# Performance work log

Hardware: AMD Instinct MI355X
Metric: run time of the kernel (lower is better)

Reference implementation:

```python
import jax, jax.numpy as jnp
import numpy as np

B, C, H, W = 4, 64, 128, 128
G, K, PAD, DIL = 4, 3, 2, 2  # deformable conv config
OFF_CH = 2 * K * K * G  # 72


def conv2d(x, w, b, pad):
    out = jax.lax.conv_general_dilated(
        x, w, window_strides=(1, 1), padding=[(pad, pad), (pad, pad)],
        dimension_numbers=('NCHW', 'OIHW', 'NCHW'))
    return out + b[None, :, None, None]


def deform_conv(x, offset, w, b):
    # DCNv1 (no modulation mask), groups=G, offset_groups=G, torchvision semantics.
    Bn, Cn, Hn, Wn = x.shape
    Cg = Cn // G
    Cout = w.shape[0]
    Coutg = Cout // G
    # offset channels laid out as [G, K*K, (dy,dx)]
    off = offset.reshape(Bn, G, K * K, 2, Hn, Wn)
    dy, dx = off[:, :, :, 0], off[:, :, :, 1]  # [B,G,9,H,W]
    kk = jnp.arange(K * K)
    gy = (jnp.arange(Hn)[None, :] - PAD + DIL * (kk // K)[:, None]).astype(x.dtype)[:, :, None]  # [9,H,1]
    gx = (jnp.arange(Wn)[None, :] - PAD + DIL * (kk % K)[:, None]).astype(x.dtype)[:, None, :]   # [9,1,W]
    py = dy + gy[None, None]  # [B,G,9,H,W]
    px = dx + gx[None, None]
    xg = x.reshape(Bn, G, Cg, Hn, Wn)

    def gather(img, py_, px_):  # img [Cg,H,W]; py_,px_ [9,H,W]
        y0 = jnp.floor(py_)
        x0 = jnp.floor(px_)
        ly = py_ - y0
        lx = px_ - x0

        def corner(iy, ix, wgt):
            valid = (iy >= 0) & (iy <= Hn - 1) & (ix >= 0) & (ix <= Wn - 1)
            iyc = jnp.clip(iy, 0, Hn - 1).astype(jnp.int32)
            ixc = jnp.clip(ix, 0, Wn - 1).astype(jnp.int32)
            return img[:, iyc, ixc] * (wgt * valid)[None]

        return (corner(y0, x0, (1 - ly) * (1 - lx))
                + corner(y0, x0 + 1, (1 - ly) * lx)
                + corner(y0 + 1, x0, ly * (1 - lx))
                + corner(y0 + 1, x0 + 1, ly * lx))

    sampled = jax.vmap(jax.vmap(gather))(xg, py, px)  # [B,G,Cg,9,H,W]
    wr = w.reshape(G, Coutg, Cg, K * K)
    out = jnp.einsum('bgckhw,gock->bgohw', sampled, wr).reshape(Bn, Cout, Hn, Wn)
    return out + b[None, :, None, None]


def setup_inputs() -> dict:
    key = jax.random.key(0)
    ks = jax.random.split(key, 32)
    f32 = jnp.float32
    d = {
        'Fref': jax.random.normal(ks[0], (B, C, H, W), f32),
        'Fmov1': jax.random.normal(ks[1], (B, C, H, W), f32),
        'Fmov2': jax.random.normal(ks[2], (B, C, H, W), f32),
        'cr_w': jax.random.normal(ks[3], (64, 128, 3, 3), f32) * 0.05,
        'cr_b': jax.random.normal(ks[4], (64,), f32) * 0.05,
    }
    i = 5
    for name in ('off1', 'off2', 'off3', 'off4'):
        d[name + '_w'] = jax.random.normal(ks[i], (OFF_CH, 64, 3, 3), f32) * 0.01
        d[name + '_b'] = jax.random.normal(ks[i + 1], (OFF_CH,), f32) * 0.01
        i += 2
    for name in ('d1', 'd2', 'd3', 'd4'):
        d[name + '_w'] = jax.random.normal(ks[i], (64, 64 // G, 3, 3), f32) * 0.05
        d[name + '_b'] = jax.random.normal(ks[i + 1], (64,), f32) * 0.05
        i += 2
    return d


def reference(Fref, Fmov1, Fmov2, cr_w, cr_b,
              off1_w, off1_b, off2_w, off2_b, off3_w, off3_b, off4_w, off4_b,
              d1_w, d1_b, d2_w, d2_b, d3_w, d3_b, d4_w, d4_b):
    def align(fr, fm):
        fea = conv2d(jnp.concatenate([fr, fm], axis=1), cr_w, cr_b, 1)
        fea = deform_conv(fea, conv2d(fea, off1_w, off1_b, 1), d1_w, d1_b)
        fea = deform_conv(fea, conv2d(fea, off2_w, off2_b, 1), d2_w, d2_b)
        off3 = conv2d(fea, off3_w, off3_b, 1)
        fea = deform_conv(fm, off3, d3_w, d3_b)  # note: deform3 applied to Fmov, per source
        out = deform_conv(fea, conv2d(fea, off4_w, off4_b, 1), d4_w, d4_b)
        return out

    return (align(Fref, Fmov1), align(Fref, Fmov2))
```

## Files before the change

kernel.cpp:

```cpp
#include <hip/hip_runtime.h>


using f16   = _Float16;
using f16x8 = __attribute__((ext_vector_type(8))) f16;
using h2    = __attribute__((ext_vector_type(2))) f16;
using u16x8 = __attribute__((ext_vector_type(8))) unsigned short;
using f32x4 = __attribute__((ext_vector_type(4))) float;

static constexpr int Hh = 128, Ww = 128, NB = 4, NPIX = Hh * Ww;
static constexpr int BB = 8;

__device__ __forceinline__ unsigned short f2h(float f) {
  f16 h = (f16)f;
  return *(unsigned short*)&h;
}

struct PrepPtrs {
  const float* cw[5];
  unsigned short* cd[5];
  const float* dw[4];
  unsigned short* dd[4];
  const float* ob[4];
  float* obd[4];
};

__global__ __launch_bounds__(256) void prep_all_kernel(PrepPtrs pp) {
  const int which = blockIdx.y;
  const int i = blockIdx.x * 256 + threadIdx.x;
  if (which == 0) {
    if (i >= 9 * 64 * 128) return;
    const int cin = 128, cop = 64;
    const int ci = i % cin, co = (i / cin) % cop, t = i / (cin * cop);
    pp.cd[0][i] = f2h(pp.cw[0][((size_t)co * cin + ci) * 9 + t]);
  } else if (which <= 4) {
    if (i >= 9 * 80 * 64) return;
    const int cin = 64, cop = 80;
    const int ci = i % cin, co = (i / cin) % cop, t = i / (cin * cop);
    const int g = co / 20, c = co % 20;
    float v = (c < 18) ? pp.cw[which][((size_t)(g * 18 + c) * cin + ci) * 9 + t]
                       : 0.f;
    pp.cd[which][i] = f2h(v);
  } else if (which <= 8) {
    if (i >= 4 * 5 * 16 * 32) return;
    const int kk = i & 31, o = (i >> 5) & 15, pair = (i >> 9) % 5;
    const int g = i / 2560;
    const int t = pair * 2 + (kk >> 4), c = kk & 15;
    float v = (t < 9) ? pp.dw[which - 5][(size_t)((g * 16 + o) * 16 + c) * 9 + t]
                      : 0.f;
    pp.dd[which - 5][i] = f2h(v);
  } else {
    if (i >= 4 * 80) return;
    const int ten = i / 80, co = i % 80;
    const int g = co / 20, c = co % 20;
    pp.obd[ten][co] = (c < 18) ? pp.ob[ten][g * 18 + c] : 0.f;
  }
}

__global__ __launch_bounds__(256) void to_gs_kernel(
    const float* __restrict__ Fref, const float* __restrict__ Fm1,
    const float* __restrict__ Fm2, unsigned short* __restrict__ frefG,
    unsigned short* __restrict__ fmovG) {
  const int t = blockIdx.x * 256 + threadIdx.x;
  const int b2 = t >> 14, pix = t & (NPIX - 1);
  const float* fm = (b2 < 4 ? Fm1 : Fm2) + (size_t)(b2 & 3) * 64 * NPIX + pix;
  for (int c8 = 0; c8 < 8; ++c8) {
    u16x8 v;
#pragma unroll
    for (int j = 0; j < 8; ++j) v[j] = f2h(fm[(size_t)(c8 * 8 + j) * NPIX]);
    *(u16x8*)(fmovG + ((size_t)(b2 * 4 + (c8 >> 1)) * NPIX + pix) * 16 +
              (c8 & 1) * 8) = v;
  }
  if (b2 < 4) {
    const float* fr = Fref + (size_t)b2 * 64 * NPIX + pix;
    for (int c8 = 0; c8 < 8; ++c8) {
      u16x8 v;
#pragma unroll
      for (int j = 0; j < 8; ++j) v[j] = f2h(fr[(size_t)(c8 * 8 + j) * NPIX]);
      *(u16x8*)(frefG + ((size_t)(b2 * 4 + (c8 >> 1)) * NPIX + pix) * 16 +
                (c8 & 1) * 8) = v;
    }
  }
}

template <int CIN, int COP, int CO_REAL>
__global__ __launch_bounds__(512, 2) void convmfma_kernel(
    const unsigned short* __restrict__ in0, int bmask0,
    const unsigned short* __restrict__ in1, int bmask1,
    const unsigned short* __restrict__ wT,
    const float* __restrict__ biasP,
    unsigned short* __restrict__ out) {
  constexpr int COF = COP / 16;
  constexpr int NCH = CIN / 64;
  constexpr int NT = NCH * 9;
  __shared__ unsigned short sW[2][COP * 64];
  __shared__ unsigned short sB[324 * 64];

  const int tile = blockIdx.x, b = blockIdx.y;
  const int ty0 = (tile >> 3) << 4, tx0 = (tile & 7) << 4;
  const int tid = threadIdx.x;
  const int wv = tid >> 6, l = tid & 63;
  const int lm = l & 15, lq = l >> 4;

  f32x4 acc[COF][2];
#pragma unroll
  for (int cf = 0; cf < COF; ++cf)
#pragma unroll
    for (int pf = 0; pf < 2; ++pf) acc[cf][pf] = (f32x4){0.f, 0.f, 0.f, 0.f};

  const unsigned short* base0 = in0 + (size_t)(b & bmask0) * 4 * NPIX * 16;
  const unsigned short* base1 =
      (NCH > 1) ? in1 + (size_t)(b & bmask1) * 4 * NPIX * 16 : nullptr;

  auto stage_input = [&](int ch) {
    const unsigned short* inB = (ch == 0) ? base0 : base1;
    for (int q = tid; q < 324 * 8; q += 512) {
      const int pix = q >> 3, ci8 = q & 7;
      const int r = pix / 18, c = pix - r * 18;
      const int gy = ty0 - 1 + r, gx = tx0 - 1 + c;
      u16x8 v;
      if (gy >= 0 && gy < Hh && gx >= 0 && gx < Ww) {
        v = *(const u16x8*)(inB + ((size_t)(ci8 >> 1) * NPIX + gy * Ww + gx) *
                                      16 + (ci8 & 1) * 8);
      } else {
#pragma unroll
        for (int j = 0; j < 8; ++j) v[j] = 0;
      }
      const int boff = pix * 128 + ((ci8 * 16) ^ ((pix & 7) << 4));
      *(u16x8*)((char*)sB + boff) = v;
    }
  };
  auto stage_w = [&](int tt, int buf) {
    const int ch = tt / 9, t = tt - ch * 9;
    for (int q = tid; q < COP * 8; q += 512) {
      const int ci8 = q & 7;
      const int co = q >> 3;
      u16x8 v = *(const u16x8*)(wT + (size_t)(t * COP + co) * CIN + ch * 64 +
                                ci8 * 8);
      const int aoff = co * 128 + ((ci8 * 16) ^ ((co & 7) << 4));
      *(u16x8*)((char*)sW[buf] + aoff) = v;
    }
  };

  stage_input(0);
  stage_w(0, 0);
  __syncthreads();

  for (int tt = 0; tt < NT; ++tt) {
    const int t = tt % 9;
    const bool nextNewCh = ((tt + 1) % 9 == 0);
    if (tt + 1 < NT && !nextNewCh) stage_w(tt + 1, (tt + 1) & 1);

    const int dy = t / 3, dx = t - dy * 3;
    const char* sWc = (const char*)sW[tt & 1];
#pragma unroll
    for (int kc = 0; kc < 2; ++kc) {
      f16x8 afr[COF];
#pragma unroll
      for (int cf = 0; cf < COF; ++cf) {
        const int co = cf * 16 + lm;
        const int aoff = co * 128 + ((kc * 64 + lq * 16) ^ ((co & 7) << 4));
        afr[cf] = *(const f16x8*)(sWc + aoff);
      }
#pragma unroll
      for (int pf = 0; pf < 2; ++pf) {
        const int pix = wv * 32 + pf * 16 + lm;
        const int spix = ((pix >> 4) + dy) * 18 + (pix & 15) + dx;
        const int boff = spix * 128 + ((kc * 64 + lq * 16) ^ ((spix & 7) << 4));
        const f16x8 bfr = *(const f16x8*)((const char*)sB + boff);
#pragma unroll
        for (int cf = 0; cf < COF; ++cf)
          acc[cf][pf] = __builtin_amdgcn_mfma_f32_16x16x32_f16(
              afr[cf], bfr, acc[cf][pf], 0, 0, 0);
      }
    }
    __syncthreads();
    if (tt + 1 < NT && nextNewCh) {
      stage_input((tt + 1) / 9);
      stage_w(tt + 1, (tt + 1) & 1);
      __syncthreads();
    }
  }

#pragma unroll
  for (int cf = 0; cf < COF; ++cf) {
    const int co0 = cf * 16 + lq * 4;
    if (co0 >= CO_REAL) continue;
    const float4 bv = *(const float4*)(biasP + co0);
#pragma unroll
    for (int pf = 0; pf < 2; ++pf) {
      const int pix = wv * 32 + pf * 16 + lm;
      const int gpix = (ty0 + (pix >> 4)) * Ww + tx0 + (pix & 15);
      const f32x4 v = acc[cf][pf];
      ushort4 pk;
      pk.x = f2h(v[0] + bv.x);
      pk.y = f2h(v[1] + bv.y);
      pk.z = f2h(v[2] + bv.z);
      pk.w = f2h(v[3] + bv.w);
      const int gg = co0 >> 4, cc = co0 & 15;
      *(ushort4*)(out + ((size_t)(b * 4 + gg) * NPIX + gpix) * 16 + cc) = pk;
    }
  }
}

template <bool NCHW_OUT>
__global__ __launch_bounds__(512, 2) void fused_od_kernel(
    const unsigned short* __restrict__ convIn,
    const unsigned short* __restrict__ sampX,
    const unsigned short* __restrict__ wT,
    const float* __restrict__ obias,
    const unsigned short* __restrict__ dwP,
    const float* __restrict__ dbias,
    float* __restrict__ outF, unsigned short* __restrict__ outH) {
  __shared__ __attribute__((aligned(16))) char lds[61952];
  unsigned short* sB = (unsigned short*)lds;
  char* sWr = lds + 41472;
  char* sOffB = lds;
  char* bounce = lds + 40960;

  const int tile = blockIdx.x, b = blockIdx.y;
  const int ty0 = (tile >> 3) << 4, tx0 = (tile & 7) << 4;
  const int tid = threadIdx.x;
  const int wv = tid >> 6, l = tid & 63;
  const int lm = l & 15, lq = l >> 4;

  f32x4 acc[5][2];
#pragma unroll
  for (int cf = 0; cf < 5; ++cf)
#pragma unroll
    for (int pf = 0; pf < 2; ++pf) acc[cf][pf] = (f32x4){0.f, 0.f, 0.f, 0.f};

  const unsigned short* inB = convIn + (size_t)b * 4 * NPIX * 16;

  for (int q = tid; q < 324 * 8; q += 512) {
    const int pix = q >> 3, ci8 = q & 7;
    const int r = pix / 18, c = pix - r * 18;
    const int gy = ty0 - 1 + r, gx = tx0 - 1 + c;
    u16x8 v;
    if (gy >= 0 && gy < Hh && gx >= 0 && gx < Ww) {
      v = *(const u16x8*)(inB + ((size_t)(ci8 >> 1) * NPIX + gy * Ww + gx) *
                                    16 + (ci8 & 1) * 8);
    } else {
#pragma unroll
      for (int j = 0; j < 8; ++j) v[j] = 0;
    }
    const int boff = pix * 128 + ((ci8 * 16) ^ ((pix & 7) << 4));
    *(u16x8*)((char*)sB + boff) = v;
  }
  auto stage_w = [&](int t, int buf) {
    for (int q = tid; q < 80 * 8; q += 512) {
      const int ci8 = q & 7;
      const int co = q >> 3;
      u16x8 v = *(const u16x8*)(wT + (size_t)(t * 80 + co) * 64 + ci8 * 8);
      const int aoff = co * 128 + ((ci8 * 16) ^ ((co & 7) << 4));
      *(u16x8*)(sWr + buf * 10240 + aoff) = v;
    }
  };
  stage_w(0, 0);
  __syncthreads();

  for (int t = 0; t < 9; ++t) {
    if (t + 1 < 9) stage_w(t + 1, (t + 1) & 1);
    const int dy = t / 3, dx = t - dy * 3;
    const char* sWc = sWr + (t & 1) * 10240;
#pragma unroll
    for (int kc = 0; kc < 2; ++kc) {
      f16x8 afr[5];
#pragma unroll
      for (int cf = 0; cf < 5; ++cf) {
        const int co = cf * 16 + lm;
        const int aoff = co * 128 + ((kc * 64 + lq * 16) ^ ((co & 7) << 4));
        afr[cf] = *(const f16x8*)(sWc + aoff);
      }
#pragma unroll
      for (int pf = 0; pf < 2; ++pf) {
        const int pix = wv * 32 + pf * 16 + lm;
        const int spix = ((pix >> 4) + dy) * 18 + (pix & 15) + dx;
        const int boff = spix * 128 + ((kc * 64 + lq * 16) ^ ((spix & 7) << 4));
        const f16x8 bfr = *(const f16x8*)((const char*)sB + boff);
#pragma unroll
        for (int cf = 0; cf < 5; ++cf)
          acc[cf][pf] = __builtin_amdgcn_mfma_f32_16x16x32_f16(
              afr[cf], bfr, acc[cf][pf], 0, 0, 0);
      }
    }
    __syncthreads();
  }

#pragma unroll
  for (int cf = 0; cf < 5; ++cf) {
    const int co0 = cf * 16 + lq * 4;
    const float4 bv = *(const float4*)(obias + co0);
#pragma unroll
    for (int pf = 0; pf < 2; ++pf) {
      const int pix = wv * 32 + pf * 16 + lm;
      const f32x4 v = acc[cf][pf];
      ushort4 pk;
      pk.x = f2h(v[0] + bv.x);
      pk.y = f2h(v[1] + bv.y);
      pk.z = f2h(v[2] + bv.z);
      pk.w = f2h(v[3] + bv.w);
      *(ushort4*)(sOffB + pix * 160 + co0 * 2) = pk;
    }
  }
  __syncthreads();

  const int p = tid >> 1, h = tid & 1;
  const int y = ty0 + (p >> 4), xx = tx0 + (p & 15);
  char* myB = bounce + p * 80 + h * 16;

  for (int g = 0; g < 4; ++g) {
    const unsigned short* xP =
        sampX + (size_t)(b * 4 + g) * NPIX * 16 + h * 8;
    unsigned od[9];
#pragma unroll
    for (int t = 0; t < 9; ++t)
      od[t] = *(const unsigned*)(sOffB + p * 160 + (g * 20 + 2 * t) * 2);

    f16x8 afr[5];
#pragma unroll
    for (int pr = 0; pr < 5; ++pr)
      afr[pr] = *(const f16x8*)(dwP + ((size_t)(g * 5 + pr) * 16 + lm) * 32 +
                                lq * 8);

    f32x4 dacc[2];
    dacc[0] = (f32x4){0.f, 0.f, 0.f, 0.f};
    dacc[1] = (f32x4){0.f, 0.f, 0.f, 0.f};

#pragma unroll
    for (int pair = 0; pair < 5; ++pair) {
#pragma unroll
      for (int ti = 0; ti < 2; ++ti) {
        const int t = pair * 2 + ti;
        uint4 sv = (uint4){0u, 0u, 0u, 0u};
        if (t < 9) {
          const unsigned odw = od[t];
          const f16* op = (const f16*)&odw;
          const float dy = (float)op[0];
          const float dx = (float)op[1];
          const float py = dy + (float)(y - 2 + 2 * (t / 3));
          const float px = dx + (float)(xx - 2 + 2 * (t % 3));
          const float fy = floorf(py), fx = floorf(px);
          const int y0 = (int)fy, x0 = (int)fx;
          const int y1 = y0 + 1, x1 = x0 + 1;
          const float ly = py - fy, lx = px - fx;
          float w00 = (1.f - ly) * (1.f - lx), w01 = (1.f - ly) * lx;
          float w10 = ly * (1.f - lx), w11 = ly * lx;
          const bool vy0 = (y0 >= 0) && (y0 < Hh), vy1 = (y1 >= 0) && (y1 < Hh);
          const bool vx0 = (x0 >= 0) && (x0 < Ww), vx1 = (x1 >= 0) && (x1 < Ww);
          w00 = (vy0 && vx0) ? w00 : 0.f;
          w01 = (vy0 && vx1) ? w01 : 0.f;
          w10 = (vy1 && vx0) ? w10 : 0.f;
          w11 = (vy1 && vx1) ? w11 : 0.f;
          const int y0c = min(max(y0, 0), Hh - 1), y1c = min(max(y1, 0), Hh - 1);
          const int x0c = min(max(x0, 0), Ww - 1), x1c = min(max(x1, 0), Ww - 1);
          const u16x8 a00 = *(const u16x8*)(xP + (size_t)(y0c * Ww + x0c) * 16);
          const u16x8 a01 = *(const u16x8*)(xP + (size_t)(y0c * Ww + x1c) * 16);
          const u16x8 a10 = *(const u16x8*)(xP + (size_t)(y1c * Ww + x0c) * 16);
          const u16x8 a11 = *(const u16x8*)(xP + (size_t)(y1c * Ww + x1c) * 16);
          const h2* c00 = (const h2*)&a00;
          const h2* c01 = (const h2*)&a01;
          const h2* c10 = (const h2*)&a10;
          const h2* c11 = (const h2*)&a11;
          const f16 h00 = (f16)w00, h01 = (f16)w01;
          const f16 h10 = (f16)w10, h11 = (f16)w11;
          const h2 p00 = (h2){h00, h00}, p01 = (h2){h01, h01};
          const h2 p10 = (h2){h10, h10}, p11 = (h2){h11, h11};
          unsigned fw[4];
#pragma unroll
          for (int j = 0; j < 4; ++j) {
            h2 r = c00[j] * p00;
            r += c01[j] * p01;
            r += c10[j] * p10;
            r += c11[j] * p11;
            fw[j] = *(const unsigned*)&r;
          }
          sv = (uint4){fw[0], fw[1], fw[2], fw[3]};
        }
        *(uint4*)(myB + ti * 32) = sv;
      }
#pragma unroll
      for (int n = 0; n < 2; ++n) {
        const f16x8 bfr =
            *(const f16x8*)(bounce + (wv * 32 + n * 16 + lm) * 80 + lq * 16);
        dacc[n] = __builtin_amdgcn_mfma_f32_16x16x32_f16(afr[pair], bfr,
                                                         dacc[n], 0, 0, 0);
      }
    }

    const float4 bv = *(const float4*)(dbias + g * 16 + lq * 4);
#pragma unroll
    for (int n = 0; n < 2; ++n) {
      const int pixl = wv * 32 + n * 16 + lm;
      const int gpix = (ty0 + (pixl >> 4)) * Ww + tx0 + (pixl & 15);
      const f32x4 v = dacc[n];
      if (NCHW_OUT) {
        float* oB = outF + (size_t)(b * 64 + g * 16 + lq * 4) * NPIX + gpix;
        oB[0] = v[0] + bv.x;
        oB[NPIX] = v[1] + bv.y;
        oB[2 * NPIX] = v[2] + bv.z;
        oB[3 * NPIX] = v[3] + bv.w;
      } else {
        ushort4 pk;
        pk.x = f2h(v[0] + bv.x);
        pk.y = f2h(v[1] + bv.y);
        pk.z = f2h(v[2] + bv.z);
        pk.w = f2h(v[3] + bv.w);
        *(ushort4*)(outH + ((size_t)(b * 4 + g) * NPIX + gpix) * 16 + lq * 4) =
            pk;
      }
    }
  }
}


extern "C" void kernel_launch(void* const* d_in, const int* in_sizes, int n_in,
                              void* d_out, int out_size, void* d_ws,
                              size_t ws_size, hipStream_t stream) {
  const float* Fref = (const float*)d_in[0];
  const float* Fmov1 = (const float*)d_in[1];
  const float* Fmov2 = (const float*)d_in[2];
  const float* cr_w = (const float*)d_in[3];
  const float* cr_b = (const float*)d_in[4];
  const float* offw[4] = {(const float*)d_in[5], (const float*)d_in[7],
                          (const float*)d_in[9], (const float*)d_in[11]};
  const float* offb[4] = {(const float*)d_in[6], (const float*)d_in[8],
                          (const float*)d_in[10], (const float*)d_in[12]};
  const float* dw[4] = {(const float*)d_in[13], (const float*)d_in[15],
                        (const float*)d_in[17], (const float*)d_in[19]};
  const float* db[4] = {(const float*)d_in[14], (const float*)d_in[16],
                        (const float*)d_in[18], (const float*)d_in[20]};

  char* p = (char*)d_ws;
  auto carve = [&](size_t bytes) {
    void* r = p;
    p += (bytes + 255) & ~(size_t)255;
    return r;
  };
  unsigned short* frefG = (unsigned short*)carve((size_t)4 * 4 * NPIX * 16 * 2);
  unsigned short* fmovG = (unsigned short*)carve((size_t)BB * 4 * NPIX * 16 * 2);
  unsigned short* feaA = (unsigned short*)carve((size_t)BB * 4 * NPIX * 16 * 2);
  unsigned short* feaB = (unsigned short*)carve((size_t)BB * 4 * NPIX * 16 * 2);
  unsigned short* wcrT = (unsigned short*)carve((size_t)9 * 64 * 128 * 2);
  unsigned short* woffT[4];
  for (int i = 0; i < 4; ++i)
    woffT[i] = (unsigned short*)carve((size_t)9 * 80 * 64 * 2);
  unsigned short* dwP[4];
  for (int i = 0; i < 4; ++i)
    dwP[i] = (unsigned short*)carve((size_t)4 * 5 * 16 * 32 * 2);
  float* obP[4];
  for (int i = 0; i < 4; ++i) obP[i] = (float*)carve((size_t)80 * 4);

  PrepPtrs pp;
  pp.cw[0] = cr_w;
  pp.cd[0] = wcrT;
  for (int i = 0; i < 4; ++i) {
    pp.cw[i + 1] = offw[i];
    pp.cd[i + 1] = woffT[i];
    pp.dw[i] = dw[i];
    pp.dd[i] = dwP[i];
    pp.ob[i] = offb[i];
    pp.obd[i] = obP[i];
  }
  prep_all_kernel<<<dim3(288, 10), 256, 0, stream>>>(pp);

  to_gs_kernel<<<BB * NPIX / 256, 256, 0, stream>>>(Fref, Fmov1, Fmov2, frefG,
                                                    fmovG);

  const dim3 fgrid(64, BB), fblk(512);
  float* outF = (float*)d_out;

  convmfma_kernel<128, 64, 64><<<fgrid, fblk, 0, stream>>>(
      frefG, 3, fmovG, 7, wcrT, cr_b, feaA);
  fused_od_kernel<false><<<fgrid, fblk, 0, stream>>>(
      feaA, feaA, woffT[0], obP[0], dwP[0], db[0], nullptr, feaB);
  fused_od_kernel<false><<<fgrid, fblk, 0, stream>>>(
      feaB, feaB, woffT[1], obP[1], dwP[1], db[1], nullptr, feaA);
  fused_od_kernel<false><<<fgrid, fblk, 0, stream>>>(
      feaA, fmovG, woffT[2], obP[2], dwP[2], db[2], nullptr, feaB);
  fused_od_kernel<true><<<fgrid, fblk, 0, stream>>>(
      feaB, feaB, woffT[3], obP[3], dwP[3], db[3], outF, nullptr);
}
```

Baseline: 239.7 us.

## Shrink fused offset/deform tiles to 4x32 with register-staged weights

The fused offset-conv plus deformable-conv kernel moves from 16x16 pixel tiles with 512 threads to 4x32 tiles with 256 threads, doubling the grid. Weight staging changes from a double-buffered LDS copy to a register prefetch followed by a single LDS buffer, with an extra barrier per tap. The offset scratch row stride is padded from 160 to 168 bytes. LDS use falls enough to fit more blocks per CU. In exchange, the 4x32 tile carries a larger halo (6x34 input rows instead of 18x18), and the added barrier per tap lengthens the serial section of the loop.

```diff
diff --git a/kernel.cpp b/kernel.cpp
--- a/kernel.cpp
+++ b/kernel.cpp
@@ -203,7 +203,7 @@
 }
 
 template <bool NCHW_OUT>
-__global__ __launch_bounds__(512, 2) void fused_od_kernel(
+__global__ __launch_bounds__(256, 4) void fused_od_kernel(
     const unsigned short* __restrict__ convIn,
     const unsigned short* __restrict__ sampX,
     const unsigned short* __restrict__ wT,
@@ -211,14 +211,15 @@
     const unsigned short* __restrict__ dwP,
     const float* __restrict__ dbias,
     float* __restrict__ outF, unsigned short* __restrict__ outH) {
-  __shared__ __attribute__((aligned(16))) char lds[61952];
-  unsigned short* sB = (unsigned short*)lds;
-  char* sWr = lds + 41472;
+  __shared__ __attribute__((aligned(16))) char lds[36352];
+  char* sB = lds;
+  char* sW = lds + 26112;
   char* sOffB = lds;
-  char* bounce = lds + 40960;
+  char* bounce = lds + 26112;
 
   const int tile = blockIdx.x, b = blockIdx.y;
-  const int ty0 = (tile >> 3) << 4, tx0 = (tile & 7) << 4;
+  const int ty0 = (tile >> 2) << 2;
+  const int tx0 = (tile & 3) << 5;
   const int tid = threadIdx.x;
   const int wv = tid >> 6, l = tid & 63;
   const int lm = l & 15, lq = l >> 4;
@@ -231,9 +232,31 @@
 
   const unsigned short* inB = convIn + (size_t)b * 4 * NPIX * 16;
 
-  for (int q = tid; q < 324 * 8; q += 512) {
+  u16x8 wr0, wr1, wr2;
+  auto wload = [&](int t) {
+    const unsigned short* wt = wT + (size_t)t * 5120;
+    wr0 = *(const u16x8*)(wt + (size_t)(tid >> 3) * 64 + (tid & 7) * 8);
+    const int q1 = tid + 256;
+    wr1 = *(const u16x8*)(wt + (size_t)(q1 >> 3) * 64 + (q1 & 7) * 8);
+    if (tid < 128) {
+      const int q2 = tid + 512;
+      wr2 = *(const u16x8*)(wt + (size_t)(q2 >> 3) * 64 + (q2 & 7) * 8);
+    }
+  };
+  auto wstore = [&]() {
+    auto put = [&](int q, u16x8 v) {
+      const int co = q >> 3, ci8 = q & 7;
+      *(u16x8*)(sW + co * 128 + ((ci8 * 16) ^ ((co & 7) << 4))) = v;
+    };
+    put(tid, wr0);
+    put(tid + 256, wr1);
+    if (tid < 128) put(tid + 512, wr2);
+  };
+
+  wload(0);
+  for (int q = tid; q < 204 * 8; q += 256) {
     const int pix = q >> 3, ci8 = q & 7;
-    const int r = pix / 18, c = pix - r * 18;
+    const int r = pix / 34, c = pix - r * 34;
     const int gy = ty0 - 1 + r, gx = tx0 - 1 + c;
     u16x8 v;
     if (gy >= 0 && gy < Hh && gx >= 0 && gx < Ww) {
@@ -244,24 +267,14 @@
       for (int j = 0; j < 8; ++j) v[j] = 0;
     }
     const int boff = pix * 128 + ((ci8 * 16) ^ ((pix & 7) << 4));
-    *(u16x8*)((char*)sB + boff) = v;
-  }
-  auto stage_w = [&](int t, int buf) {
-    for (int q = tid; q < 80 * 8; q += 512) {
-      const int ci8 = q & 7;
-      const int co = q >> 3;
-      u16x8 v = *(const u16x8*)(wT + (size_t)(t * 80 + co) * 64 + ci8 * 8);
-      const int aoff = co * 128 + ((ci8 * 16) ^ ((co & 7) << 4));
-      *(u16x8*)(sWr + buf * 10240 + aoff) = v;
-    }
-  };
-  stage_w(0, 0);
+    *(u16x8*)(sB + boff) = v;
+  }
+  wstore();
   __syncthreads();
 
   for (int t = 0; t < 9; ++t) {
-    if (t + 1 < 9) stage_w(t + 1, (t + 1) & 1);
+    if (t + 1 < 9) wload(t + 1);
     const int dy = t / 3, dx = t - dy * 3;
-    const char* sWc = sWr + (t & 1) * 10240;
 #pragma unroll
     for (int kc = 0; kc < 2; ++kc) {
       f16x8 afr[5];
@@ -269,14 +282,14 @@
       for (int cf = 0; cf < 5; ++cf) {
         const int co = cf * 16 + lm;
         const int aoff = co * 128 + ((kc * 64 + lq * 16) ^ ((co & 7) << 4));
-        afr[cf] = *(const f16x8*)(sWc + aoff);
+        afr[cf] = *(const f16x8*)(sW + aoff);
       }
 #pragma unroll
       for (int pf = 0; pf < 2; ++pf) {
         const int pix = wv * 32 + pf * 16 + lm;
-        const int spix = ((pix >> 4) + dy) * 18 + (pix & 15) + dx;
+        const int spix = ((pix >> 5) + dy) * 34 + (pix & 31) + dx;
         const int boff = spix * 128 + ((kc * 64 + lq * 16) ^ ((spix & 7) << 4));
-        const f16x8 bfr = *(const f16x8*)((const char*)sB + boff);
+        const f16x8 bfr = *(const f16x8*)(sB + boff);
 #pragma unroll
         for (int cf = 0; cf < 5; ++cf)
           acc[cf][pf] = __builtin_amdgcn_mfma_f32_16x16x32_f16(
@@ -284,6 +297,10 @@
       }
     }
     __syncthreads();
+    if (t + 1 < 9) {
+      wstore();
+      __syncthreads();
+    }
   }
 
 #pragma unroll
@@ -299,13 +316,13 @@
       pk.y = f2h(v[1] + bv.y);
       pk.z = f2h(v[2] + bv.z);
       pk.w = f2h(v[3] + bv.w);
-      *(ushort4*)(sOffB + pix * 160 + co0 * 2) = pk;
+      *(ushort4*)(sOffB + pix * 168 + co0 * 2) = pk;
     }
   }
   __syncthreads();
 
   const int p = tid >> 1, h = tid & 1;
-  const int y = ty0 + (p >> 4), xx = tx0 + (p & 15);
+  const int y = ty0 + (p >> 5), xx = tx0 + (p & 31);
   char* myB = bounce + p * 80 + h * 16;
 
   for (int g = 0; g < 4; ++g) {
@@ -314,7 +331,7 @@
     unsigned od[9];
 #pragma unroll
     for (int t = 0; t < 9; ++t)
-      od[t] = *(const unsigned*)(sOffB + p * 160 + (g * 20 + 2 * t) * 2);
+      od[t] = *(const unsigned*)(sOffB + p * 168 + (g * 20 + 2 * t) * 2);
 
     f16x8 afr[5];
 #pragma unroll
@@ -391,7 +408,7 @@
 #pragma unroll
     for (int n = 0; n < 2; ++n) {
       const int pixl = wv * 32 + n * 16 + lm;
-      const int gpix = (ty0 + (pixl >> 4)) * Ww + tx0 + (pixl & 15);
+      const int gpix = (ty0 + (pixl >> 5)) * Ww + tx0 + (pixl & 31);
       const f32x4 v = dacc[n];
       if (NCHW_OUT) {
         float* oB = outF + (size_t)(b * 64 + g * 16 + lq * 4) * NPIX + gpix;
@@ -466,10 +483,11 @@
   to_gs_kernel<<<BB * NPIX / 256, 256, 0, stream>>>(Fref, Fmov1, Fmov2, frefG,
                                                     fmovG);
 
-  const dim3 fgrid(64, BB), fblk(512);
+  const dim3 cgrid(64, BB), cblk(512);
+  const dim3 fgrid(128, BB), fblk(256);
   float* outF = (float*)d_out;
 
-  convmfma_kernel<128, 64, 64><<<fgrid, fblk, 0, stream>>>(
+  convmfma_kernel<128, 64, 64><<<cgrid, cblk, 0, stream>>>(
       frefG, 3, fmovG, 7, wcrT, cr_b, feaA);
   fused_od_kernel<false><<<fgrid, fblk, 0, stream>>>(
       feaA, feaA, woffT[0], obP[0], dwP[0], db[0], nullptr, feaB);
```

Result: no change. 235.7 us (-1.7%).
